# Kernel optimization log

Measured on AMD Instinct MI355X. Metric: run time of the kernel, lower is better.

## Reference

```python
import jax, jax.numpy as jnp
import numpy as np

N_NODES = 100000
N_EDGES = 1600000
N_QEDGES = 400000
NUM_FEAT = 128
HIDDEN_C = 128
OUT_C = 64
NO_HEADS = 8


def setup_inputs() -> dict:
    key = jax.random.key(0)
    ks = jax.random.split(key, 8)
    x = jax.random.normal(ks[0], (N_NODES, NUM_FEAT), dtype=jnp.float32)
    W1 = jax.random.normal(ks[1], (NUM_FEAT, HIDDEN_C), dtype=jnp.float32) * (1.0 / np.sqrt(NUM_FEAT))
    b1 = jnp.zeros((HIDDEN_C,), dtype=jnp.float32)
    W2 = jax.random.normal(ks[2], (HIDDEN_C, OUT_C * NO_HEADS), dtype=jnp.float32) * (1.0 / np.sqrt(HIDDEN_C))
    b2 = jnp.zeros((OUT_C * NO_HEADS,), dtype=jnp.float32)
    edge_index = jax.random.randint(ks[3], (2, N_EDGES), 0, N_NODES, dtype=jnp.int32)
    q_edge_index = jax.random.randint(ks[4], (2, N_QEDGES), 0, N_NODES, dtype=jnp.int32)
    y = jax.random.randint(ks[5], (N_NODES,), 0, NO_HEADS, dtype=jnp.int32)
    return {"x": x, "W1": W1, "b1": b1, "W2": W2, "b2": b2,
            "edge_index": edge_index, "q_edge_index": q_edge_index, "y": y}


def gcn_conv(x, W, b, src, dst, n):
    """GCNConv: symmetric normalization with implicit self-loops."""
    h = x @ W  # [n, out]
    ones = jnp.ones(src.shape[0], dtype=x.dtype)
    deg = jax.ops.segment_sum(ones, dst, num_segments=n) + 1.0  # self-loop
    dinv = jax.lax.rsqrt(deg)
    norm = dinv[src] * dinv[dst]  # [E]
    agg = jax.ops.segment_sum(h[src] * norm[:, None], dst, num_segments=n)
    agg = agg + h * (dinv * dinv)[:, None]  # self-loop message
    return agg + b


def reference(x, W1, b1, W2, b2, edge_index, q_edge_index, y):
    src, dst = edge_index[0], edge_index[1]
    n = x.shape[0]
    hiddens = jax.nn.relu(gcn_conv(x, W1, b1, src, dst, n))            # [N, H]
    emb = gcn_conv(hiddens, W2, b2, src, dst, n)                        # [N, heads*out]
    emb = emb.reshape(n, NO_HEADS, OUT_C)                               # [N, h, f]
    q_row, q_col = q_edge_index[0], q_edge_index[1]
    preds = jnp.einsum('ehf,ehf->eh', emb[q_row], emb[q_col])           # [Q, h]
    pred_i = jnp.take_along_axis(preds, y[q_row][:, None].astype(jnp.int32), axis=1)[:, 0]
    pred_j = jnp.take_along_axis(preds, y[q_col][:, None].astype(jnp.int32), axis=1)[:, 0]
    pred = (pred_i + pred_j) * 0.5  # multiheads=True branch
    return hiddens, emb, pred_i, pred_j, pred
```

## Files before the change

kernel.cpp:

```cpp
#include <hip/hip_runtime.h>
#include <hip/hip_bf16.h>


#define SCAN_SEG 512

typedef short bf16x8 __attribute__((ext_vector_type(8)));
typedef float f32x4  __attribute__((ext_vector_type(4)));

__device__ __forceinline__ ushort f2bf(float x) {
    return (ushort)(__float_as_uint(x) >> 16);
}
__device__ __forceinline__ float bf2f(ushort h) {
    return __uint_as_float(((unsigned)h) << 16);
}

__global__ void count_kernel(const int* __restrict__ dst, int* __restrict__ cnt, int E) {
    int e = blockIdx.x * blockDim.x + threadIdx.x;
    if (e < E) atomicAdd(&cnt[dst[e]], 1);
}

__global__ __launch_bounds__(256) void blocksum_kernel(const int* __restrict__ cnt,
                                                       int* __restrict__ blocksum, int n) {
    __shared__ int red[4];
    int b = blockIdx.x, t = threadIdx.x;
    int i0 = b * SCAN_SEG + t;
    int s = 0;
    if (i0 < n) s += cnt[i0];
    if (i0 + 256 < n) s += cnt[i0 + 256];
#pragma unroll
    for (int off = 32; off >= 1; off >>= 1) s += __shfl_xor(s, off, 64);
    if ((t & 63) == 0) red[t >> 6] = s;
    __syncthreads();
    if (t == 0) blocksum[b] = red[0] + red[1] + red[2] + red[3];
}

__global__ __launch_bounds__(256) void blockscan_kernel(const int* __restrict__ blocksum,
                                                        int* __restrict__ blockoff, int nb,
                                                        int* __restrict__ row_ptr, int n, int E) {
    __shared__ int s[256];
    int t = threadIdx.x;
    int v = (t < nb) ? blocksum[t] : 0;
    s[t] = v;
    __syncthreads();
    for (int off = 1; off < 256; off <<= 1) {
        int u = (t >= off) ? s[t - off] : 0;
        __syncthreads();
        s[t] += u;
        __syncthreads();
    }
    if (t < nb) blockoff[t] = s[t] - v;
    if (t == 0) row_ptr[n] = E;
}

__global__ __launch_bounds__(256) void csr_ptr_kernel(const int* __restrict__ cnt,
                                                      const int* __restrict__ blockoff,
                                                      int* __restrict__ row_ptr,
                                                      int* __restrict__ cursor,
                                                      float* __restrict__ dinv, int n) {
    __shared__ int s[256];
    int b = blockIdx.x, t = threadIdx.x;
    int i0 = b * SCAN_SEG + 2 * t;
    int c0 = (i0     < n) ? cnt[i0]     : 0;
    int c1 = (i0 + 1 < n) ? cnt[i0 + 1] : 0;
    int pair = c0 + c1;
    s[t] = pair;
    __syncthreads();
    for (int off = 1; off < 256; off <<= 1) {
        int u = (t >= off) ? s[t - off] : 0;
        __syncthreads();
        s[t] += u;
        __syncthreads();
    }
    int excl = s[t] - pair + blockoff[b];
    if (i0 < n) {
        row_ptr[i0] = excl;
        cursor[i0]  = excl;
        dinv[i0]    = rsqrtf((float)(c0 + 1));
    }
    if (i0 + 1 < n) {
        row_ptr[i0 + 1] = excl + c0;
        cursor[i0 + 1]  = excl + c0;
        dinv[i0 + 1]    = rsqrtf((float)(c1 + 1));
    }
}

__global__ void fill_kernel(const int* __restrict__ src, const int* __restrict__ dst,
                            int* __restrict__ cursor, const float* __restrict__ dinv,
                            int* __restrict__ csr_src, float* __restrict__ csr_wt, int E) {
    int e = blockIdx.x * blockDim.x + threadIdx.x;
    if (e < E) {
        int s = src[e], d = dst[e];
        int pos = atomicAdd(&cursor[d], 1);
        csr_src[pos] = s;
        csr_wt[pos]  = dinv[s] * dinv[d];
    }
}

__global__ __launch_bounds__(256) void wsplit_kernel(const float* __restrict__ W,
                                                     ushort* __restrict__ th,
                                                     ushort* __restrict__ tl, int ncols) {
    int idx = blockIdx.x * 256 + threadIdx.x;
    if (idx >= 128 * ncols) return;
    int col = idx >> 7;
    int k   = idx & 127;
    float v = W[(size_t)k * ncols + col];
    ushort h = f2bf(v);
    th[idx] = h;
    tl[idx] = f2bf(v - bf2f(h));
}

__global__ __launch_bounds__(256) void agg_kernel(const float* __restrict__ feat,
                                                  const int* __restrict__ row_ptr,
                                                  const int* __restrict__ csr_src,
                                                  const float* __restrict__ csr_wt,
                                                  const float* __restrict__ dinv,
                                                  ushort* __restrict__ outh,
                                                  ushort* __restrict__ outl, int n) {
    const int w    = threadIdx.x >> 6;
    const int lane = threadIdx.x & 63;
    const int node = blockIdx.x * 4 + w;
    if (node >= n) return;
    const int g = lane >> 5;
    const int c = lane & 31;

    float di = dinv[node];
    float4 acc = make_float4(0.f, 0.f, 0.f, 0.f);
    if (g == 0) {
        float4 v = ((const float4*)(feat + (size_t)node * 128))[c];
        float s2 = di * di;
        acc.x = v.x * s2; acc.y = v.y * s2; acc.z = v.z * s2; acc.w = v.w * s2;
    }

    int e0 = row_ptr[node], e1 = row_ptr[node + 1];
    int e = e0 + g;
    for (; e + 2 < e1; e += 4) {
        int   s0 = csr_src[e],  s1 = csr_src[e + 2];
        float w0 = csr_wt[e],   w1 = csr_wt[e + 2];
        float4 v0 = ((const float4*)(feat + (size_t)s0 * 128))[c];
        float4 v1 = ((const float4*)(feat + (size_t)s1 * 128))[c];
        acc.x += v0.x * w0 + v1.x * w1;
        acc.y += v0.y * w0 + v1.y * w1;
        acc.z += v0.z * w0 + v1.z * w1;
        acc.w += v0.w * w0 + v1.w * w1;
    }
    for (; e < e1; e += 2) {
        int   s0 = csr_src[e];
        float w0 = csr_wt[e];
        float4 v0 = ((const float4*)(feat + (size_t)s0 * 128))[c];
        acc.x += v0.x * w0; acc.y += v0.y * w0; acc.z += v0.z * w0; acc.w += v0.w * w0;
    }

    acc.x += __shfl_xor(acc.x, 32, 64);
    acc.y += __shfl_xor(acc.y, 32, 64);
    acc.z += __shfl_xor(acc.z, 32, 64);
    acc.w += __shfl_xor(acc.w, 32, 64);

    if (g == 0) {
        ushort4 h, l;
        h.x = f2bf(acc.x); l.x = f2bf(acc.x - bf2f(h.x));
        h.y = f2bf(acc.y); l.y = f2bf(acc.y - bf2f(h.y));
        h.z = f2bf(acc.z); l.z = f2bf(acc.z - bf2f(h.z));
        h.w = f2bf(acc.w); l.w = f2bf(acc.w - bf2f(h.w));
        *(ushort4*)(outh + (size_t)node * 128 + c * 4) = h;
        *(ushort4*)(outl + (size_t)node * 128 + c * 4) = l;
    }
}

__global__ __launch_bounds__(256, 2) void gemm_mfma(const ushort* __restrict__ Xh_g,
                                                    const ushort* __restrict__ Xl_g,
                                                    const ushort* __restrict__ Wth_g,
                                                    const ushort* __restrict__ Wtl_g,
                                                    const float* __restrict__ bias,
                                                    float* __restrict__ C,
                                                    int N, int ldw, int do_relu) {
    __shared__ ushort Xh[128 * 64];
    __shared__ ushort Xl[128 * 64];
    __shared__ ushort Wh[128 * 64];
    __shared__ ushort Wl[128 * 64];

    const int tid  = threadIdx.x;
    const int lane = tid & 63;
    const int wv   = tid >> 6;
    const int wr   = wv >> 1;
    const int wc   = wv & 1;
    const int lr   = lane & 15;
    const int lk   = lane >> 4;
    const int row0   = blockIdx.y * 128;
    const int colOff = blockIdx.x * 128;

    f32x4 acc[4][4];
#pragma unroll
    for (int i = 0; i < 4; ++i)
#pragma unroll
        for (int j = 0; j < 4; ++j)
            acc[i][j] = (f32x4){0.f, 0.f, 0.f, 0.f};

    for (int ph = 0; ph < 2; ++ph) {
        if (ph) __syncthreads();

#pragma unroll
        for (int q = 0; q < 4; ++q) {
            int cidx = tid + 256 * q;
            int row  = cidx >> 3;
            int kch  = cidx & 7;
            int gr   = row0 + row; if (gr >= N) gr = N - 1;
            size_t ge = (size_t)gr * 128 + ph * 64 + kch * 8;
            int lb = row * 128 + ((kch * 16) ^ ((row & 7) << 4));
            *(int4*)((char*)Xh + lb) = *(const int4*)(Xh_g + ge);
            *(int4*)((char*)Xl + lb) = *(const int4*)(Xl_g + ge);
        }
#pragma unroll
        for (int q = 0; q < 4; ++q) {
            int cidx = tid + 256 * q;
            int col  = cidx >> 3;
            int kch  = cidx & 7;
            size_t ge = (size_t)(colOff + col) * 128 + ph * 64 + kch * 8;
            int lb = col * 128 + ((kch * 16) ^ ((col & 7) << 4));
            *(int4*)((char*)Wh + lb) = *(const int4*)(Wth_g + ge);
            *(int4*)((char*)Wl + lb) = *(const int4*)(Wtl_g + ge);
        }
        __syncthreads();

#pragma unroll
        for (int kk = 0; kk < 2; ++kk) {
            const int kb2 = (kk * 32 + lk * 8) * 2;
            bf16x8 ah[4], al[4], bh[4], bl[4];
#pragma unroll
            for (int mi = 0; mi < 4; ++mi) {
                int row  = wr * 64 + mi * 16 + lr;
                int byte = row * 128 + (kb2 ^ ((row & 7) << 4));
                ah[mi] = *(const bf16x8*)((const char*)Xh + byte);
                al[mi] = *(const bf16x8*)((const char*)Xl + byte);
            }
#pragma unroll
            for (int ni = 0; ni < 4; ++ni) {
                int col  = wc * 64 + ni * 16 + lr;
                int byte = col * 128 + (kb2 ^ ((col & 7) << 4));
                bh[ni] = *(const bf16x8*)((const char*)Wh + byte);
                bl[ni] = *(const bf16x8*)((const char*)Wl + byte);
            }
#pragma unroll
            for (int mi = 0; mi < 4; ++mi)
#pragma unroll
                for (int ni = 0; ni < 4; ++ni) {
                    acc[mi][ni] = __builtin_amdgcn_mfma_f32_16x16x32_bf16(
                        ah[mi], bh[ni], acc[mi][ni], 0, 0, 0);
                    acc[mi][ni] = __builtin_amdgcn_mfma_f32_16x16x32_bf16(
                        ah[mi], bl[ni], acc[mi][ni], 0, 0, 0);
                    acc[mi][ni] = __builtin_amdgcn_mfma_f32_16x16x32_bf16(
                        al[mi], bh[ni], acc[mi][ni], 0, 0, 0);
                }
        }
    }

#pragma unroll
    for (int ni = 0; ni < 4; ++ni) {
        int col = colOff + wc * 64 + ni * 16 + lr;
        float bv = bias[col];
#pragma unroll
        for (int mi = 0; mi < 4; ++mi) {
            int rbase = row0 + wr * 64 + mi * 16 + (lane >> 4) * 4;
#pragma unroll
            for (int r = 0; r < 4; ++r) {
                int row = rbase + r;
                if (row < N) {
                    float v = acc[mi][ni][r] + bv;
                    if (do_relu) v = fmaxf(v, 0.f);
                    C[(size_t)row * ldw + col] = v;
                }
            }
        }
    }
}

__global__ __launch_bounds__(256) void query_kernel(const float* __restrict__ emb,
                                                    const int* __restrict__ qrow,
                                                    const int* __restrict__ qcol,
                                                    const int* __restrict__ y,
                                                    float* __restrict__ pred_i,
                                                    float* __restrict__ pred_j,
                                                    float* __restrict__ pred, int Q) {
    int wave = (int)((blockIdx.x * 256 + threadIdx.x) >> 6);
    int lane = threadIdx.x & 63;
    if (wave >= Q) return;
    int r = qrow[wave], c = qcol[wave];
    int yr = y[r], yc = y[c];
    int g = lane >> 4;
    int t = lane & 15;
    int node = (g & 1) ? c : r;
    int head = (g >> 1) ? yc : yr;
    const float4* p = (const float4*)(emb + (size_t)node * 512 + head * 64);
    float4 v = p[t];
    float4 o;
    o.x = __shfl_xor(v.x, 16, 64);
    o.y = __shfl_xor(v.y, 16, 64);
    o.z = __shfl_xor(v.z, 16, 64);
    o.w = __shfl_xor(v.w, 16, 64);
    float s = v.x * o.x + v.y * o.y + v.z * o.z + v.w * o.w;
#pragma unroll
    for (int off = 8; off >= 1; off >>= 1) s += __shfl_xor(s, off, 64);
    float other = __shfl_xor(s, 32, 64);
    if (lane == 0) {
        pred_i[wave] = s;
        pred_j[wave] = other;
        pred[wave]   = 0.5f * (s + other);
    }
}

extern "C" void kernel_launch(void* const* d_in, const int* in_sizes, int n_in,
                              void* d_out, int out_size, void* d_ws, size_t ws_size,
                              hipStream_t stream) {
    const float* x   = (const float*)d_in[0];
    const float* W1  = (const float*)d_in[1];
    const float* b1  = (const float*)d_in[2];
    const float* W2  = (const float*)d_in[3];
    const float* b2  = (const float*)d_in[4];
    const int* edge  = (const int*)d_in[5];
    const int* qedge = (const int*)d_in[6];
    const int* y     = (const int*)d_in[7];

    const int N = in_sizes[0] / 128;
    const int E = in_sizes[5] / 2;
    const int Q = in_sizes[6] / 2;

    float* out     = (float*)d_out;
    float* hiddens = out;
    float* emb     = out + (size_t)N * 128;
    float* pred_i  = emb + (size_t)N * 512;
    float* pred_j  = pred_i + Q;
    float* pred    = pred_j + Q;

    char* w = (char*)d_ws;
    auto alloc = [&](size_t bytes) { char* p = w; w += (bytes + 255) & ~(size_t)255; return p; };
    int*    cnt      = (int*)alloc((size_t)N * 4);
    int*    row_ptr  = (int*)alloc((size_t)(N + 1) * 4);
    int*    cursor   = (int*)alloc((size_t)N * 4);
    float*  dinv     = (float*)alloc((size_t)N * 4);
    int*    csr_src  = (int*)alloc((size_t)E * 4);
    float*  csr_wt   = (float*)alloc((size_t)E * 4);
    int*    blocksum = (int*)alloc(256 * 4);
    int*    blockoff = (int*)alloc(256 * 4);
    ushort* aggh     = (ushort*)alloc((size_t)N * 128 * 2);
    ushort* aggl     = (ushort*)alloc((size_t)N * 128 * 2);
    ushort* w1h      = (ushort*)alloc(128 * 128 * 2);
    ushort* w1l      = (ushort*)alloc(128 * 128 * 2);
    ushort* w2h      = (ushort*)alloc(128 * 512 * 2);
    ushort* w2l      = (ushort*)alloc(128 * 512 * 2);

    const int* esrc = edge;         const int* edst = edge + E;
    const int* qrow = qedge;        const int* qcol = qedge + Q;

    const int nb = (N + SCAN_SEG - 1) / SCAN_SEG;

    hipMemsetAsync(cnt, 0, (size_t)N * 4, stream);
    count_kernel<<<dim3((E + 255) / 256), dim3(256), 0, stream>>>(edst, cnt, E);
    blocksum_kernel<<<dim3(nb), dim3(256), 0, stream>>>(cnt, blocksum, N);
    blockscan_kernel<<<dim3(1), dim3(256), 0, stream>>>(blocksum, blockoff, nb, row_ptr, N, E);
    csr_ptr_kernel<<<dim3(nb), dim3(256), 0, stream>>>(cnt, blockoff, row_ptr, cursor, dinv, N);
    fill_kernel<<<dim3((E + 255) / 256), dim3(256), 0, stream>>>(esrc, edst, cursor, dinv, csr_src, csr_wt, E);

    wsplit_kernel<<<dim3((128 * 128 + 255) / 256), dim3(256), 0, stream>>>(W1, w1h, w1l, 128);
    wsplit_kernel<<<dim3((128 * 512 + 255) / 256), dim3(256), 0, stream>>>(W2, w2h, w2l, 512);

    const int mblocks = (N + 127) / 128;
    const int ablocks = (N + 3) / 4;

    agg_kernel<<<dim3(ablocks), dim3(256), 0, stream>>>(x, row_ptr, csr_src, csr_wt, dinv, aggh, aggl, N);
    gemm_mfma<<<dim3(1, mblocks), dim3(256), 0, stream>>>(aggh, aggl, w1h, w1l, b1, hiddens, N, 128, 1);

    agg_kernel<<<dim3(ablocks), dim3(256), 0, stream>>>(hiddens, row_ptr, csr_src, csr_wt, dinv, aggh, aggl, N);
    gemm_mfma<<<dim3(4, mblocks), dim3(256), 0, stream>>>(aggh, aggl, w2h, w2l, b2, emb, N, 512, 0);

    query_kernel<<<dim3((Q + 3) / 4), dim3(256), 0, stream>>>(emb, qrow, qcol, y, pred_i, pred_j, pred, Q);
}
```

Baseline: 945.8 us.

## Factor GCN normalization into prescaled features and drop per-edge weights

Splits the symmetric normalization dinv[s]*dinv[d] into a source-side prescale of the feature rows and a destination-side scale applied once after aggregation. The per-edge weight array and its loads disappear, and the edge loop becomes plain sums with deeper unrolling and a contiguous half-split per wave half. The first GEMM epilogue now also writes a dinv-scaled copy of hiddens, and a new prescale pass handles x. The cost is an extra N×128 float buffer plus an extra write in the GEMM and the prescale kernel, which raises memory traffic in exchange for lighter gathers.

```diff
diff --git a/kernel.cpp b/kernel.cpp
--- a/kernel.cpp
+++ b/kernel.cpp
@@ -85,15 +85,25 @@
 }
 
 __global__ void fill_kernel(const int* __restrict__ src, const int* __restrict__ dst,
-                            int* __restrict__ cursor, const float* __restrict__ dinv,
-                            int* __restrict__ csr_src, float* __restrict__ csr_wt, int E) {
+                            int* __restrict__ cursor, int* __restrict__ csr_src, int E) {
     int e = blockIdx.x * blockDim.x + threadIdx.x;
     if (e < E) {
-        int s = src[e], d = dst[e];
+        int d = dst[e];
         int pos = atomicAdd(&cursor[d], 1);
-        csr_src[pos] = s;
-        csr_wt[pos]  = dinv[s] * dinv[d];
-    }
+        csr_src[pos] = src[e];
+    }
+}
+
+__global__ __launch_bounds__(256) void prescale_kernel(const float* __restrict__ x,
+                                                       const float* __restrict__ dinv,
+                                                       float* __restrict__ xs, int n) {
+    int id = blockIdx.x * 256 + threadIdx.x;
+    if (id >= n * 32) return;
+    int row = id >> 5;
+    float di = dinv[row];
+    float4 v = ((const float4*)x)[id];
+    v.x *= di; v.y *= di; v.z *= di; v.w *= di;
+    ((float4*)xs)[id] = v;
 }
 
 __global__ __launch_bounds__(256) void wsplit_kernel(const float* __restrict__ W,
@@ -112,7 +122,6 @@
 __global__ __launch_bounds__(256) void agg_kernel(const float* __restrict__ feat,
                                                   const int* __restrict__ row_ptr,
                                                   const int* __restrict__ csr_src,
-                                                  const float* __restrict__ csr_wt,
                                                   const float* __restrict__ dinv,
                                                   ushort* __restrict__ outh,
                                                   ushort* __restrict__ outl, int n) {
@@ -123,44 +132,63 @@
     const int g = lane >> 5;
     const int c = lane & 31;
 
-    float di = dinv[node];
-    float4 acc = make_float4(0.f, 0.f, 0.f, 0.f);
-    if (g == 0) {
-        float4 v = ((const float4*)(feat + (size_t)node * 128))[c];
-        float s2 = di * di;
-        acc.x = v.x * s2; acc.y = v.y * s2; acc.z = v.z * s2; acc.w = v.w * s2;
-    }
-
-    int e0 = row_ptr[node], e1 = row_ptr[node + 1];
-    int e = e0 + g;
-    for (; e + 2 < e1; e += 4) {
-        int   s0 = csr_src[e],  s1 = csr_src[e + 2];
-        float w0 = csr_wt[e],   w1 = csr_wt[e + 2];
+    const float di = dinv[node];
+    float4 acc0 = make_float4(0.f, 0.f, 0.f, 0.f);
+    float4 acc1 = make_float4(0.f, 0.f, 0.f, 0.f);
+    if (g == 0)
+        acc0 = ((const float4*)(feat + (size_t)node * 128))[c];
+
+    const int e0 = row_ptr[node], e1 = row_ptr[node + 1];
+    const int half = (e1 - e0 + 1) >> 1;
+    int e  = e0 + (g ? half : 0);
+    const int ge = g ? e1 : e0 + half;
+
+    for (; e + 7 < ge; e += 8) {
+        int s0 = csr_src[e],     s1 = csr_src[e + 1];
+        int s2 = csr_src[e + 2], s3 = csr_src[e + 3];
+        int s4 = csr_src[e + 4], s5 = csr_src[e + 5];
+        int s6 = csr_src[e + 6], s7 = csr_src[e + 7];
         float4 v0 = ((const float4*)(feat + (size_t)s0 * 128))[c];
         float4 v1 = ((const float4*)(feat + (size_t)s1 * 128))[c];
-        acc.x += v0.x * w0 + v1.x * w1;
-        acc.y += v0.y * w0 + v1.y * w1;
-        acc.z += v0.z * w0 + v1.z * w1;
-        acc.w += v0.w * w0 + v1.w * w1;
-    }
-    for (; e < e1; e += 2) {
-        int   s0 = csr_src[e];
-        float w0 = csr_wt[e];
+        float4 v2 = ((const float4*)(feat + (size_t)s2 * 128))[c];
+        float4 v3 = ((const float4*)(feat + (size_t)s3 * 128))[c];
+        float4 v4 = ((const float4*)(feat + (size_t)s4 * 128))[c];
+        float4 v5 = ((const float4*)(feat + (size_t)s5 * 128))[c];
+        float4 v6 = ((const float4*)(feat + (size_t)s6 * 128))[c];
+        float4 v7 = ((const float4*)(feat + (size_t)s7 * 128))[c];
+        acc0.x += v0.x + v2.x + v4.x + v6.x;  acc1.x += v1.x + v3.x + v5.x + v7.x;
+        acc0.y += v0.y + v2.y + v4.y + v6.y;  acc1.y += v1.y + v3.y + v5.y + v7.y;
+        acc0.z += v0.z + v2.z + v4.z + v6.z;  acc1.z += v1.z + v3.z + v5.z + v7.z;
+        acc0.w += v0.w + v2.w + v4.w + v6.w;  acc1.w += v1.w + v3.w + v5.w + v7.w;
+    }
+    for (; e + 1 < ge; e += 2) {
+        int s0 = csr_src[e], s1 = csr_src[e + 1];
         float4 v0 = ((const float4*)(feat + (size_t)s0 * 128))[c];
-        acc.x += v0.x * w0; acc.y += v0.y * w0; acc.z += v0.z * w0; acc.w += v0.w * w0;
-    }
-
-    acc.x += __shfl_xor(acc.x, 32, 64);
-    acc.y += __shfl_xor(acc.y, 32, 64);
-    acc.z += __shfl_xor(acc.z, 32, 64);
-    acc.w += __shfl_xor(acc.w, 32, 64);
+        float4 v1 = ((const float4*)(feat + (size_t)s1 * 128))[c];
+        acc0.x += v0.x; acc1.x += v1.x;
+        acc0.y += v0.y; acc1.y += v1.y;
+        acc0.z += v0.z; acc1.z += v1.z;
+        acc0.w += v0.w; acc1.w += v1.w;
+    }
+    if (e < ge) {
+        int s0 = csr_src[e];
+        float4 v0 = ((const float4*)(feat + (size_t)s0 * 128))[c];
+        acc0.x += v0.x; acc0.y += v0.y; acc0.z += v0.z; acc0.w += v0.w;
+    }
+    acc0.x += acc1.x; acc0.y += acc1.y; acc0.z += acc1.z; acc0.w += acc1.w;
+
+    acc0.x += __shfl_xor(acc0.x, 32, 64);
+    acc0.y += __shfl_xor(acc0.y, 32, 64);
+    acc0.z += __shfl_xor(acc0.z, 32, 64);
+    acc0.w += __shfl_xor(acc0.w, 32, 64);
 
     if (g == 0) {
+        acc0.x *= di; acc0.y *= di; acc0.z *= di; acc0.w *= di;
         ushort4 h, l;
-        h.x = f2bf(acc.x); l.x = f2bf(acc.x - bf2f(h.x));
-        h.y = f2bf(acc.y); l.y = f2bf(acc.y - bf2f(h.y));
-        h.z = f2bf(acc.z); l.z = f2bf(acc.z - bf2f(h.z));
-        h.w = f2bf(acc.w); l.w = f2bf(acc.w - bf2f(h.w));
+        h.x = f2bf(acc0.x); l.x = f2bf(acc0.x - bf2f(h.x));
+        h.y = f2bf(acc0.y); l.y = f2bf(acc0.y - bf2f(h.y));
+        h.z = f2bf(acc0.z); l.z = f2bf(acc0.z - bf2f(h.z));
+        h.w = f2bf(acc0.w); l.w = f2bf(acc0.w - bf2f(h.w));
         *(ushort4*)(outh + (size_t)node * 128 + c * 4) = h;
         *(ushort4*)(outl + (size_t)node * 128 + c * 4) = l;
     }
@@ -172,6 +200,8 @@
                                                     const ushort* __restrict__ Wtl_g,
                                                     const float* __restrict__ bias,
                                                     float* __restrict__ C,
+                                                    float* __restrict__ hs,
+                                                    const float* __restrict__ dinvp,
                                                     int N, int ldw, int do_relu) {
     __shared__ ushort Xh[128 * 64];
     __shared__ ushort Xl[128 * 64];
@@ -267,6 +297,7 @@
                     float v = acc[mi][ni][r] + bv;
                     if (do_relu) v = fmaxf(v, 0.f);
                     C[(size_t)row * ldw + col] = v;
+                    if (hs) hs[(size_t)row * 128 + col] = v * dinvp[row];
                 }
             }
         }
@@ -337,9 +368,9 @@
     int*    cursor   = (int*)alloc((size_t)N * 4);
     float*  dinv     = (float*)alloc((size_t)N * 4);
     int*    csr_src  = (int*)alloc((size_t)E * 4);
-    float*  csr_wt   = (float*)alloc((size_t)E * 4);
     int*    blocksum = (int*)alloc(256 * 4);
     int*    blockoff = (int*)alloc(256 * 4);
+    float*  scaled   = (float*)alloc((size_t)N * 128 * 4);
     ushort* aggh     = (ushort*)alloc((size_t)N * 128 * 2);
     ushort* aggl     = (ushort*)alloc((size_t)N * 128 * 2);
     ushort* w1h      = (ushort*)alloc(128 * 128 * 2);
@@ -357,7 +388,8 @@
     blocksum_kernel<<<dim3(nb), dim3(256), 0, stream>>>(cnt, blocksum, N);
     blockscan_kernel<<<dim3(1), dim3(256), 0, stream>>>(blocksum, blockoff, nb, row_ptr, N, E);
     csr_ptr_kernel<<<dim3(nb), dim3(256), 0, stream>>>(cnt, blockoff, row_ptr, cursor, dinv, N);
-    fill_kernel<<<dim3((E + 255) / 256), dim3(256), 0, stream>>>(esrc, edst, cursor, dinv, csr_src, csr_wt, E);
+    prescale_kernel<<<dim3((N * 32 + 255) / 256), dim3(256), 0, stream>>>(x, dinv, scaled, N);
+    fill_kernel<<<dim3((E + 255) / 256), dim3(256), 0, stream>>>(esrc, edst, cursor, csr_src, E);
 
     wsplit_kernel<<<dim3((128 * 128 + 255) / 256), dim3(256), 0, stream>>>(W1, w1h, w1l, 128);
     wsplit_kernel<<<dim3((128 * 512 + 255) / 256), dim3(256), 0, stream>>>(W2, w2h, w2l, 512);
@@ -365,11 +397,13 @@
     const int mblocks = (N + 127) / 128;
     const int ablocks = (N + 3) / 4;
 
-    agg_kernel<<<dim3(ablocks), dim3(256), 0, stream>>>(x, row_ptr, csr_src, csr_wt, dinv, aggh, aggl, N);
-    gemm_mfma<<<dim3(1, mblocks), dim3(256), 0, stream>>>(aggh, aggl, w1h, w1l, b1, hiddens, N, 128, 1);
-
-    agg_kernel<<<dim3(ablocks), dim3(256), 0, stream>>>(hiddens, row_ptr, csr_src, csr_wt, dinv, aggh, aggl, N);
-    gemm_mfma<<<dim3(4, mblocks), dim3(256), 0, stream>>>(aggh, aggl, w2h, w2l, b2, emb, N, 512, 0);
+    agg_kernel<<<dim3(ablocks), dim3(256), 0, stream>>>(scaled, row_ptr, csr_src, dinv, aggh, aggl, N);
+    gemm_mfma<<<dim3(1, mblocks), dim3(256), 0, stream>>>(aggh, aggl, w1h, w1l, b1, hiddens,
+                                                          scaled , dinv, N, 128, 1);
+
+    agg_kernel<<<dim3(ablocks), dim3(256), 0, stream>>>(scaled, row_ptr, csr_src, dinv, aggh, aggl, N);
+    gemm_mfma<<<dim3(4, mblocks), dim3(256), 0, stream>>>(aggh, aggl, w2h, w2l, b2, emb,
+                                                          nullptr, nullptr, N, 512, 0);
 
     query_kernel<<<dim3((Q + 3) / 4), dim3(256), 0, stream>>>(emb, qrow, qcol, y, pred_i, pred_j, pred, Q);
 }
```

After: 991.4 us. 1.05x slower.
